# Optimization experiments

Measured on AMD Instinct MI355X. Metric: run time of the kernel, lower is better.

Reference implementation:

```python
import jax, jax.numpy as jnp
import numpy as np

N, D = 4096, 784

def _conv_relu(x, w, b):
    y = jax.lax.conv_general_dilated(x, w, window_strides=(1, 1), padding='SAME',
                                     dimension_numbers=('NHWC', 'HWIO', 'NHWC'))
    return jax.nn.relu(y + b)

def _maxpool2(x):
    return jax.lax.reduce_window(x, -jnp.inf, jax.lax.max,
                                 (1, 2, 2, 1), (1, 2, 2, 1), 'SAME')

def _encoder(x, cw1, cb1, cw2, cb2, cw3, cb3, dw, db):
    h = x.reshape(-1, 28, 28, 1)
    h = _maxpool2(_conv_relu(h, cw1, cb1))   # [N,14,14,32]
    h = _maxpool2(_conv_relu(h, cw2, cb2))   # [N,7,7,32]
    h = _conv_relu(h, cw3, cb3)              # [N,7,7,16]
    h = h.reshape(h.shape[0], -1)            # [N,784]
    return h @ dw + db                       # [N,16]

def _pairwise_dist(a):
    # Euclidean cdist via Gram trick; avoids the O(N^2 * D) broadcasted diff.
    sq = jnp.sum(a * a, axis=-1)
    d2 = sq[:, None] + sq[None, :] - 2.0 * (a @ a.T)
    return jnp.sqrt(jnp.maximum(d2, 1e-12))

def setup_inputs() -> dict:
    key = jax.random.key(0)
    ks = jax.random.split(key, 5)
    return {
        'x':   jax.random.uniform(ks[0], (N, D), dtype=jnp.float32),
        'cw1': jax.random.normal(ks[1], (3, 3, 1, 32), dtype=jnp.float32) * 0.1,
        'cb1': jnp.zeros((32,), jnp.float32),
        'cw2': jax.random.normal(ks[2], (3, 3, 32, 32), dtype=jnp.float32) * 0.05,
        'cb2': jnp.zeros((32,), jnp.float32),
        'cw3': jax.random.normal(ks[3], (3, 3, 32, 16), dtype=jnp.float32) * 0.05,
        'cb3': jnp.zeros((16,), jnp.float32),
        'dw':  jax.random.normal(ks[4], (D, 16), dtype=jnp.float32) * 0.05,
        'db':  jnp.zeros((16,), jnp.float32),
        'nnfactor': 64,
    }

def reference(x, cw1, cb1, cw2, cb2, cw3, cb3, dw, db, nnfactor):
    n = x.shape[0]
    k = n // nnfactor  # as in train_step
    encoded = _encoder(x, cw1, cb1, cw2, cb2, cw3, cb3, dw, db)
    # tensor_get_nearest (faithful: tf.nn.top_k takes LARGEST distances)
    d_ini = _pairwise_dist(x)                       # [N,N]
    vals_ini, idx = jax.lax.top_k(d_ini, k - 1)     # sorted descending
    vals_ini = vals_ini[:, 1:]                      # [N,k-2]
    idx = idx[:, 1:]
    d_enc = _pairwise_dist(encoded)                 # [N,N]
    vals_enc = jnp.take_along_axis(d_enc, idx, axis=1)
    multiple = jnp.mean(vals_ini / vals_enc)
    reduced = vals_enc * multiple
    # per-row custom loss: max squared error, then mean over batch
    losses = jnp.max(jnp.square(vals_ini - reduced), axis=1)  # [N]
    total_loss = jnp.sum(losses) / n
    return total_loss
```

## Files before the change

### kernel.cpp

```cpp
#include <hip/hip_runtime.h>
#include <math.h>

#define NN 4096
#define DIM 784
#define K62 62
#define CAP 160
#define NEED 80u

typedef __attribute__((ext_vector_type(8))) short bf16x8;
typedef __attribute__((ext_vector_type(4))) float f32x4;

__global__ __launch_bounds__(256) void k_sqnorm(const float* __restrict__ x, double* __restrict__ sqnd,
                                                float* __restrict__ sqnf) {
    int r = blockIdx.x * 4 + (threadIdx.x >> 6);
    int lane = threadIdx.x & 63;
    const float* xr = x + (size_t)r * DIM;
    double s = 0.0;
    for (int k = lane; k < DIM; k += 64) { double v = (double)xr[k]; s += v * v; }
    for (int o = 32; o > 0; o >>= 1) s += __shfl_down(s, o);
    if (lane == 0) { sqnd[r] = s; sqnf[r] = (float)s; }
}

#define F4C(v, i) ((i) == 0 ? (v).x : (i) == 1 ? (v).y : (i) == 2 ? (v).z : (v).w)

__device__ __forceinline__ unsigned short f2bf(float f) {
    unsigned u = __float_as_uint(f);
    return (unsigned short)((u + 0x7FFFu + ((u >> 16) & 1u)) >> 16);
}

__global__ __launch_bounds__(256) void k_tobf16(const float* __restrict__ x, unsigned short* __restrict__ xb) {
    int idx = blockIdx.x * 256 + threadIdx.x;
    int r = idx / 200;
    int c = (idx - r * 200) * 4;
    ushort4 o;
    if (c < DIM) {
        float4 v = *(const float4*)(x + (size_t)r * DIM + c);
        o.x = f2bf(v.x); o.y = f2bf(v.y); o.z = f2bf(v.z); o.w = f2bf(v.w);
    } else {
        o.x = 0; o.y = 0; o.z = 0; o.w = 0;
    }
    *(ushort4*)(xb + (size_t)r * 800 + c) = o;
}

__global__ __launch_bounds__(256, 2) void k_gram_mfma(const unsigned short* __restrict__ xb,
                                                      const float* __restrict__ sqnf,
                                                      unsigned short* __restrict__ Dm16) {
    __shared__ unsigned short Cs16[64 * 72];
    int t = threadIdx.x;
    int id = blockIdx.x;
    int bi = (int)((sqrtf(8.f * (float)id + 1.f) - 1.f) * 0.5f);
    while ((bi + 1) * (bi + 2) / 2 <= id) ++bi;
    while (bi * (bi + 1) / 2 > id) --bi;
    int bj = id - bi * (bi + 1) / 2;
    int i0 = bi * 128, j0 = bj * 128;
    int wv = t >> 6, ln = t & 63;
    int l16 = ln & 15, kg = ln >> 4;

    f32x4 acc[2][8];
    #pragma unroll
    for (int rt = 0; rt < 2; ++rt)
    #pragma unroll
    for (int ct = 0; ct < 8; ++ct)
    #pragma unroll
    for (int e = 0; e < 4; ++e) acc[rt][ct][e] = 0.f;

    const unsigned short* arow0 = xb + (size_t)(i0 + wv * 32 + l16) * 800 + kg * 8;
    const unsigned short* arow1 = arow0 + 16 * 800;
    const unsigned short* brow  = xb + (size_t)(j0 + l16) * 800 + kg * 8;

    for (int ks = 0; ks < 25; ++ks) {
        bf16x8 a0 = *(const bf16x8*)(arow0 + ks * 32);
        bf16x8 a1 = *(const bf16x8*)(arow1 + ks * 32);
        #pragma unroll
        for (int ct = 0; ct < 8; ++ct) {
            bf16x8 b = *(const bf16x8*)(brow + (size_t)ct * 16 * 800 + ks * 32);
            acc[0][ct] = __builtin_amdgcn_mfma_f32_16x16x32_bf16(a0, b, acc[0][ct], 0, 0, 0);
            acc[1][ct] = __builtin_amdgcn_mfma_f32_16x16x32_bf16(a1, b, acc[1][ct], 0, 0, 0);
        }
    }
    #pragma unroll
    for (int rt = 0; rt < 2; ++rt) {
        int gr0 = i0 + wv * 32 + rt * 16 + kg * 4;
        #pragma unroll
        for (int ct = 0; ct < 8; ++ct) {
            int gc = j0 + ct * 16 + l16;
            float sj = sqnf[gc];
            #pragma unroll
            for (int j = 0; j < 4; ++j) {
                float d2 = fmaxf(sqnf[gr0 + j] + sj - 2.f * acc[rt][ct][j], 1e-12f);
                Dm16[(size_t)(gr0 + j) * NN + gc] = (unsigned short)(__float_as_uint(d2) >> 16);
            }
        }
    }
    if (bi != bj) {
        for (int qr = 0; qr < 2; ++qr)
        for (int qc = 0; qc < 2; ++qc) {
            __syncthreads();
            #pragma unroll
            for (int g = 0; g < 2; ++g) {
                int idx = t + g * 256;
                int a = idx >> 3, c8 = idx & 7;
                uint4 v = *(const uint4*)&Dm16[(size_t)(i0 + qr * 64 + a) * NN + j0 + qc * 64 + c8 * 8];
                Cs16[(c8 * 8 + 0) * 72 + a] = (unsigned short)(v.x);
                Cs16[(c8 * 8 + 1) * 72 + a] = (unsigned short)(v.x >> 16);
                Cs16[(c8 * 8 + 2) * 72 + a] = (unsigned short)(v.y);
                Cs16[(c8 * 8 + 3) * 72 + a] = (unsigned short)(v.y >> 16);
                Cs16[(c8 * 8 + 4) * 72 + a] = (unsigned short)(v.z);
                Cs16[(c8 * 8 + 5) * 72 + a] = (unsigned short)(v.z >> 16);
                Cs16[(c8 * 8 + 6) * 72 + a] = (unsigned short)(v.w);
                Cs16[(c8 * 8 + 7) * 72 + a] = (unsigned short)(v.w >> 16);
            }
            __syncthreads();
            #pragma unroll
            for (int g = 0; g < 2; ++g) {
                int idx = t + g * 256;
                int a = idx >> 3, c8 = idx & 7;
                uint4 v = *(const uint4*)&Cs16[a * 72 + c8 * 8];
                *(uint4*)&Dm16[(size_t)(j0 + qc * 64 + a) * NN + i0 + qr * 64 + c8 * 8] = v;
            }
        }
    }
}

__global__ __launch_bounds__(256, 4) void k_encoder(const float* __restrict__ x,
    const float* __restrict__ cw1, const float* __restrict__ cb1,
    const float* __restrict__ cw2, const float* __restrict__ cb2,
    const float* __restrict__ cw3, const float* __restrict__ cb3,
    const float* __restrict__ dw, const float* __restrict__ db,
    double* __restrict__ Enc, double* __restrict__ esqd)
{
    __shared__ __align__(16) unsigned char SB[17408];
    float*  sb1  = (float*)(SB);
    float*  sb2  = (float*)(SB + 128);
    float*  sb3  = (float*)(SB + 256);
    float*  sdb  = (float*)(SB + 320);
    float*  scw1 = (float*)(SB + 384);
    float*  wq   = (float*)(SB + 1536);
    float*  simg = (float*)(SB + 6144);
    float*  h1q  = (float*)(SB + 9744);
    float*  wq3  = (float*)(SB + 1536);
    float*  h2s  = (float*)(SB + 6144);
    float*  c3   = (float*)(SB + 6144);
    double* red  = (double*)(SB + 14768);
    double* se   = (double*)(SB + 16816);

    int t = threadIdx.x;
    int n = blockIdx.x;
    for (int idx = t; idx < 1280; idx += 256) h1q[idx] = 0.f;
    for (int idx = t; idx < 900; idx += 256) simg[idx] = 0.f;
    __syncthreads();
    if (t < 196) {
        int row = t / 7, c4 = t % 7;
        float4 v = ((const float4*)(x + (size_t)n * DIM))[t];
        float* d = &simg[(row + 1) * 30 + 1 + c4 * 4];
        d[0] = v.x; d[1] = v.y; d[2] = v.z; d[3] = v.w;
    }
    for (int idx = t; idx < 288; idx += 256) scw1[idx] = cw1[idx];
    if (t < 32) { sb1[t] = cb1[t]; sb2[t] = cb2[t]; }
    if (t < 16) { sb3[t] = cb3[t]; sdb[t] = db[t]; }
    __syncthreads();

    int p2 = t >> 2, co8 = (t & 3) * 8;
    int py2 = p2 / 7, px2 = p2 % 7;
    int cbase = ((2 * py2) * 16 + 2 * px2) * 5;
    int ch1 = t & 3;
    float acc[4][8];
    if (t < 196) {
        #pragma unroll
        for (int pp = 0; pp < 4; ++pp)
        #pragma unroll
        for (int q = 0; q < 8; ++q) acc[pp][q] = sb2[co8 + q];
    }

    for (int oct = 0; oct < 8; ++oct) {
        __syncthreads();
        {
            int co = (oct << 2) + ch1;
            float wv[9];
            #pragma unroll
            for (int tp = 0; tp < 9; ++tp) wv[tp] = scw1[tp * 32 + co];
            float bias = sb1[co];
            for (int o = t; o < 784; o += 256) {
                int p = o >> 2;
                int py = p / 14, px = p % 14;
                float m = 0.f;
                #pragma unroll
                for (int dy = 0; dy < 2; ++dy)
                #pragma unroll
                for (int dx = 0; dx < 2; ++dx) {
                    const float* sp = &simg[(2 * py + dy + 1) * 30 + (2 * px + dx + 1)];
                    float a = bias;
                    a = fmaf(sp[-31], wv[0], a);
                    a = fmaf(sp[-30], wv[1], a);
                    a = fmaf(sp[-29], wv[2], a);
                    a = fmaf(sp[ -1], wv[3], a);
                    a = fmaf(sp[  0], wv[4], a);
                    a = fmaf(sp[  1], wv[5], a);
                    a = fmaf(sp[ 29], wv[6], a);
                    a = fmaf(sp[ 30], wv[7], a);
                    a = fmaf(sp[ 31], wv[8], a);
                    if (a < 0.f) a = 0.f;
                    if (a > m) m = a;
                }
                h1q[((py + 1) * 16 + (px + 1)) * 5 + ch1] = m;
            }
        }
        for (int w2 = t; w2 < 1152; w2 += 256) {
            int tap = w2 >> 7, k = w2 & 127;
            wq[w2] = cw2[tap * 1024 + oct * 128 + k];
        }
        __syncthreads();
        if (t < 196) {
            #pragma unroll
            for (int ky = 0; ky < 3; ++ky)
            #pragma unroll
            for (int kx = 0; kx < 3; ++kx) {
                const float* wb0 = &wq[(ky * 3 + kx) * 128 + co8];
                const float* hb = &h1q[cbase + (ky * 16 + kx) * 5];
                #pragma unroll
                for (int ci = 0; ci < 4; ++ci) {
                    float4 wA = *(const float4*)(wb0 + ci * 32);
                    float4 wB = *(const float4*)(wb0 + ci * 32 + 4);
                    float v00 = hb[ci];
                    float v01 = hb[5 + ci];
                    float v10 = hb[80 + ci];
                    float v11 = hb[85 + ci];
                    acc[0][0] = fmaf(v00, wA.x, acc[0][0]); acc[0][1] = fmaf(v00, wA.y, acc[0][1]);
                    acc[0][2] = fmaf(v00, wA.z, acc[0][2]); acc[0][3] = fmaf(v00, wA.w, acc[0][3]);
                    acc[0][4] = fmaf(v00, wB.x, acc[0][4]); acc[0][5] = fmaf(v00, wB.y, acc[0][5]);
                    acc[0][6] = fmaf(v00, wB.z, acc[0][6]); acc[0][7] = fmaf(v00, wB.w, acc[0][7]);
                    acc[1][0] = fmaf(v01, wA.x, acc[1][0]); acc[1][1] = fmaf(v01, wA.y, acc[1][1]);
                    acc[1][2] = fmaf(v01, wA.z, acc[1][2]); acc[1][3] = fmaf(v01, wA.w, acc[1][3]);
                    acc[1][4] = fmaf(v01, wB.x, acc[1][4]); acc[1][5] = fmaf(v01, wB.y, acc[1][5]);
                    acc[1][6] = fmaf(v01, wB.z, acc[1][6]); acc[1][7] = fmaf(v01, wB.w, acc[1][7]);
                    acc[2][0] = fmaf(v10, wA.x, acc[2][0]); acc[2][1] = fmaf(v10, wA.y, acc[2][1]);
                    acc[2][2] = fmaf(v10, wA.z, acc[2][2]); acc[2][3] = fmaf(v10, wA.w, acc[2][3]);
                    acc[2][4] = fmaf(v10, wB.x, acc[2][4]); acc[2][5] = fmaf(v10, wB.y, acc[2][5]);
                    acc[2][6] = fmaf(v10, wB.z, acc[2][6]); acc[2][7] = fmaf(v10, wB.w, acc[2][7]);
                    acc[3][0] = fmaf(v11, wA.x, acc[3][0]); acc[3][1] = fmaf(v11, wA.y, acc[3][1]);
                    acc[3][2] = fmaf(v11, wA.z, acc[3][2]); acc[3][3] = fmaf(v11, wA.w, acc[3][3]);
                    acc[3][4] = fmaf(v11, wB.x, acc[3][4]); acc[3][5] = fmaf(v11, wB.y, acc[3][5]);
                    acc[3][6] = fmaf(v11, wB.z, acc[3][6]); acc[3][7] = fmaf(v11, wB.w, acc[3][7]);
                }
            }
        }
    }
    __syncthreads();
    if (t < 196) {
        float mm[8];
        #pragma unroll
        for (int q = 0; q < 8; ++q) {
            float m = 0.f;
            #pragma unroll
            for (int pp = 0; pp < 4; ++pp) {
                float a = acc[pp][q];
                if (a < 0.f) a = 0.f;
                if (a > m) m = a;
            }
            mm[q] = m;
        }
        *(float4*)&h2s[p2 * 44 + co8]     = make_float4(mm[0], mm[1], mm[2], mm[3]);
        *(float4*)&h2s[p2 * 44 + co8 + 4] = make_float4(mm[4], mm[5], mm[6], mm[7]);
    }
    float a0 = 0.f, a1 = 0.f, a2 = 0.f, a3 = 0.f;
    int p3 = t >> 2, co4 = (t & 3) * 4;
    int py3 = p3 / 7, px3 = p3 % 7;
    if (t < 196) {
        a0 = sb3[co4]; a1 = sb3[co4 + 1];
        a2 = sb3[co4 + 2]; a3 = sb3[co4 + 3];
    }
    for (int qq = 0; qq < 4; ++qq) {
        __syncthreads();
        for (int w2 = t; w2 < 1152; w2 += 256) {
            int tap = w2 >> 7, k = w2 & 127;
            wq3[w2] = cw3[tap * 512 + qq * 128 + k];
        }
        __syncthreads();
        if (t < 196) {
            for (int ky = 0; ky < 3; ++ky) {
                int iy = py3 + ky - 1; if ((unsigned)iy >= 7u) continue;
                for (int kx = 0; kx < 3; ++kx) {
                    int ix = px3 + kx - 1; if ((unsigned)ix >= 7u) continue;
                    const float* hp = &h2s[(iy * 7 + ix) * 44 + qq * 8];
                    float4 h0 = *(const float4*)hp;
                    float4 h1 = *(const float4*)(hp + 4);
                    const float* wp = &wq3[(ky * 3 + kx) * 128 + co4];
                    #pragma unroll
                    for (int ci = 0; ci < 8; ++ci) {
                        float av = (ci < 4) ? F4C(h0, ci) : F4C(h1, ci - 4);
                        float4 wv = *(const float4*)(wp + ci * 16);
                        a0 = fmaf(av, wv.x, a0); a1 = fmaf(av, wv.y, a1);
                        a2 = fmaf(av, wv.z, a2); a3 = fmaf(av, wv.w, a3);
                    }
                }
            }
        }
    }
    __syncthreads();
    if (t < 196) {
        float r0 = a0 > 0.f ? a0 : 0.f, r1 = a1 > 0.f ? a1 : 0.f;
        float r2 = a2 > 0.f ? a2 : 0.f, r3 = a3 > 0.f ? a3 : 0.f;
        *(float4*)&c3[p3 * 16 + co4] = make_float4(r0, r1, r2, r3);
    }
    __syncthreads();
    {
        int part = t >> 4, o = t & 15, j0 = part * 49;
        double s = 0.0;
        for (int j = 0; j < 49; ++j) s = fma((double)c3[j0 + j], (double)dw[(size_t)(j0 + j) * 16 + o], s);
        red[part * 16 + o] = s;
    }
    __syncthreads();
    if (t < 16) {
        double e = (double)sdb[t];
        for (int q = 0; q < 16; ++q) e += red[q * 16 + t];
        Enc[(size_t)n * 16 + t] = e;
        se[t] = e;
    }
    __syncthreads();
    if (t == 0) {
        double s = 0.0;
        for (int q = 0; q < 16; ++q) s += se[q] * se[q];
        esqd[n] = s;
    }
}

__global__ __launch_bounds__(256) void k_topsel(const unsigned short* __restrict__ Dm16,
                                                const double* __restrict__ sqnd,
                                                const float* __restrict__ x,
                                                double* __restrict__ topvd, int* __restrict__ topi) {
    __shared__ float xi[DIM];
    __shared__ unsigned wsum[8];
    __shared__ int cj[CAP];
    __shared__ double cvd[CAP];
    __shared__ unsigned ncnt;
    int i = blockIdx.x, t = threadIdx.x;
    const unsigned* drow = (const unsigned*)(Dm16 + (size_t)i * NN);
    unsigned uk[8];
    #pragma unroll
    for (int s = 0; s < 8; ++s) {
        int wd = t + s * 256;
        unsigned u = drow[wd];
        if (2 * wd == i)     u &= 0xFFFF0000u;
        if (2 * wd + 1 == i) u &= 0x0000FFFFu;
        uk[s] = u;
    }
    if (t < 196) ((float4*)xi)[t] = ((const float4*)(x + (size_t)i * DIM))[t];
    if (t == 0) ncnt = 0;
    int lane = t & 63, w = t >> 6;
    unsigned lo = 0u, hi = 0xFFFFu;
    for (int it = 0; it < 16; ++it) {
        unsigned mid = (lo + hi + 1u) >> 1;
        unsigned cnt = 0;
        #pragma unroll
        for (int s = 0; s < 8; ++s) {
            cnt += ((uk[s] & 0xFFFFu) >= mid) ? 1u : 0u;
            cnt += ((uk[s] >> 16) >= mid) ? 1u : 0u;
        }
        #pragma unroll
        for (int off = 32; off > 0; off >>= 1) cnt += __shfl_down(cnt, off);
        if (lane == 0) wsum[(it & 1) * 4 + w] = cnt;
        __syncthreads();
        int bb = (it & 1) * 4;
        unsigned tot = wsum[bb] + wsum[bb + 1] + wsum[bb + 2] + wsum[bb + 3];
        if (tot >= NEED) lo = mid; else hi = mid - 1u;
    }
    unsigned prefix = lo;
    #pragma unroll
    for (int s = 0; s < 8; ++s) {
        int wd = t + s * 256;
        if ((uk[s] & 0xFFFFu) >= prefix) {
            unsigned p = atomicAdd(&ncnt, 1u);
            if (p < CAP) cj[p] = 2 * wd;
        }
        if ((uk[s] >> 16) >= prefix) {
            unsigned p = atomicAdd(&ncnt, 1u);
            if (p < CAP) cj[p] = 2 * wd + 1;
        }
    }
    __syncthreads();
    int ncand = min((int)ncnt, CAP);
    double sqi_d = sqnd[i];
    const float4* xi4 = (const float4*)xi;
    int g = t >> 4, gl = t & 15;
    for (int c = g; c < ncand; c += 16) {
        const float4* xj4 = (const float4*)(x + (size_t)cj[c] * DIM);
        double s = 0.0;
        for (int k = gl; k < 196; k += 16) {
            float4 a = xi4[k]; float4 b = xj4[k];
            s = fma((double)a.x, (double)b.x, s);
            s = fma((double)a.y, (double)b.y, s);
            s = fma((double)a.z, (double)b.z, s);
            s = fma((double)a.w, (double)b.w, s);
        }
        #pragma unroll
        for (int o = 8; o > 0; o >>= 1) s += __shfl_down(s, o, 16);
        if (gl == 0) cvd[c] = sqrt(fmax(sqi_d + sqnd[cj[c]] - 2.0 * s, 1e-12));
    }
    __syncthreads();
    if (t < ncand) {
        double v = cvd[t]; int jj = cj[t];
        int r = 0;
        for (int c2 = 0; c2 < ncand; ++c2) {
            double v2 = cvd[c2];
            if (v2 > v || (v2 == v && cj[c2] < jj)) ++r;
        }
        if (r >= 1 && r < 63) {
            topvd[(size_t)i * K62 + r - 1] = v;
            topi[(size_t)i * K62 + r - 1] = jj;
        }
    }
}

__global__ __launch_bounds__(256) void k_ratio(const double* __restrict__ Enc, const double* __restrict__ esqd,
                                               const double* __restrict__ topvd, const int* __restrict__ topi,
                                               double* __restrict__ vencd, double* __restrict__ Sp) {
    __shared__ double wp[4];
    int r = blockIdx.x * 4 + (threadIdx.x >> 6);
    int lane = threadIdx.x & 63, w = threadIdx.x >> 6;
    double ratio = 0.0;
    if (lane < K62) {
        int j = topi[(size_t)r * K62 + lane];
        const double* Er = Enc + (size_t)r * 16;
        const double* Ej = Enc + (size_t)j * 16;
        double dot = 0.0;
        #pragma unroll
        for (int q = 0; q < 16; ++q) dot = fma(Er[q], Ej[q], dot);
        double ve = sqrt(fmax(esqd[r] + esqd[j] - 2.0 * dot, 1e-12));
        vencd[(size_t)r * K62 + lane] = ve;
        ratio = topvd[(size_t)r * K62 + lane] / ve;
    }
    for (int o = 32; o > 0; o >>= 1) ratio += __shfl_down(ratio, o);
    if (lane == 0) wp[w] = ratio;
    __syncthreads();
    if (threadIdx.x == 0) Sp[blockIdx.x] = wp[0] + wp[1] + wp[2] + wp[3];
}

__global__ __launch_bounds__(256) void k_loss(const double* __restrict__ topvd, const double* __restrict__ vencd,
                                              const double* __restrict__ Sp, double* __restrict__ Lp) {
    __shared__ double wp[4];
    __shared__ double wq2[4];
    int t = threadIdx.x;
    int lane = t & 63, w = t >> 6;
    double sp = Sp[t] + Sp[t + 256] + Sp[t + 512] + Sp[t + 768];
    for (int o = 32; o > 0; o >>= 1) sp += __shfl_down(sp, o);
    if (lane == 0) wp[w] = sp;
    __syncthreads();
    double m = (wp[0] + wp[1] + wp[2] + wp[3]) * (1.0 / (4096.0 * 62.0));
    int r = blockIdx.x * 4 + w;
    double v = -1.0;
    if (lane < K62) {
        double d = topvd[(size_t)r * K62 + lane] - m * vencd[(size_t)r * K62 + lane];
        v = d * d;
    }
    for (int o = 32; o > 0; o >>= 1) { double ov = __shfl_down(v, o); v = (ov > v) ? ov : v; }
    if (lane == 0) wq2[w] = v;
    __syncthreads();
    if (t == 0) Lp[blockIdx.x] = wq2[0] + wq2[1] + wq2[2] + wq2[3];
}

__global__ __launch_bounds__(256) void k_final(const double* __restrict__ Lp, float* __restrict__ out) {
    __shared__ double wp[4];
    int t = threadIdx.x, lane = t & 63, w = t >> 6;
    double s = Lp[t] + Lp[t + 256] + Lp[t + 512] + Lp[t + 768];
    for (int o = 32; o > 0; o >>= 1) s += __shfl_down(s, o);
    if (lane == 0) wp[w] = s;
    __syncthreads();
    if (t == 0) out[0] = (float)((wp[0] + wp[1] + wp[2] + wp[3]) * (1.0 / 4096.0));
}

extern "C" void kernel_launch(void* const* d_in, const int* in_sizes, int n_in,
                              void* d_out, int out_size, void* d_ws, size_t ws_size,
                              hipStream_t stream) {
    const float* x   = (const float*)d_in[0];
    const float* cw1 = (const float*)d_in[1];
    const float* cb1 = (const float*)d_in[2];
    const float* cw2 = (const float*)d_in[3];
    const float* cb2 = (const float*)d_in[4];
    const float* cw3 = (const float*)d_in[5];
    const float* cb3 = (const float*)d_in[6];
    const float* dw  = (const float*)d_in[7];
    const float* db  = (const float*)d_in[8];

    char* wsb = (char*)d_ws;
    unsigned short* Dm16 = (unsigned short*)wsb;
    double* Enc   = (double*)(wsb + 33554432);
    double* esqd  = (double*)(wsb + 34078720);
    double* sqnd  = (double*)(wsb + 34111488);
    float*  sqnf  = (float*)(wsb + 34144256);
    double* topvd = (double*)(wsb + 34160640);
    double* vencd = (double*)(wsb + 36192256);
    int*    topi  = (int*)(wsb + 38223872);
    double* Sp    = (double*)(wsb + 39239680);
    double* Lp    = (double*)(wsb + 39247872);
    unsigned short* xb = (unsigned short*)(wsb + 39256064);
    float*  out   = (float*)d_out;

    k_sqnorm<<<1024, 256, 0, stream>>>(x, sqnd, sqnf);
    k_tobf16<<<3200, 256, 0, stream>>>(x, xb);
    k_gram_mfma<<<528, 256, 0, stream>>>(xb, sqnf, Dm16);
    k_encoder<<<4096, 256, 0, stream>>>(x, cw1, cb1, cw2, cb2, cw3, cb3, dw, db, Enc, esqd);
    k_topsel<<<4096, 256, 0, stream>>>(Dm16, sqnd, x, topvd, topi);
    k_ratio<<<1024, 256, 0, stream>>>(Enc, esqd, topvd, topi, vencd, Sp);
    k_loss<<<1024, 256, 0, stream>>>(topvd, vencd, Sp, Lp);
    k_final<<<1, 256, 0, stream>>>(Lp, out);
}
```

Before: 572.2 us.

## Fuse sqnorm with bf16 conversion and process two images per encoder block

Merges the squared-norm and bf16-conversion kernels into one pass over x, removing a launch and a second read of the input. The encoder now runs 512-thread blocks that each handle two images, sharing the staged conv2/conv3 weight loads between both halves and halving the number of weight copies into shared memory. This raises shared memory per block and makes each barrier wait on twice as many threads, which may reduce occupancy. The fused prep kernel uses scalar 2-byte stores in place of the earlier vectorized ushort4 stores.

```diff
diff --git a/kernel.cpp b/kernel.cpp
--- a/kernel.cpp
+++ b/kernel.cpp
@@ -10,37 +10,32 @@
 typedef __attribute__((ext_vector_type(8))) short bf16x8;
 typedef __attribute__((ext_vector_type(4))) float f32x4;
 
-__global__ __launch_bounds__(256) void k_sqnorm(const float* __restrict__ x, double* __restrict__ sqnd,
-                                                float* __restrict__ sqnf) {
+__device__ __forceinline__ unsigned short f2bf(float f) {
+    unsigned u = __float_as_uint(f);
+    return (unsigned short)((u + 0x7FFFu + ((u >> 16) & 1u)) >> 16);
+}
+
+__global__ __launch_bounds__(256) void k_prep(const float* __restrict__ x, double* __restrict__ sqnd,
+                                              float* __restrict__ sqnf, unsigned short* __restrict__ xb) {
     int r = blockIdx.x * 4 + (threadIdx.x >> 6);
     int lane = threadIdx.x & 63;
     const float* xr = x + (size_t)r * DIM;
+    unsigned short* xbr = xb + (size_t)r * 800;
     double s = 0.0;
-    for (int k = lane; k < DIM; k += 64) { double v = (double)xr[k]; s += v * v; }
+    for (int k = lane; k < 800; k += 64) {
+        if (k < DIM) {
+            float v = xr[k];
+            s = fma((double)v, (double)v, s);
+            xbr[k] = f2bf(v);
+        } else {
+            xbr[k] = 0;
+        }
+    }
     for (int o = 32; o > 0; o >>= 1) s += __shfl_down(s, o);
     if (lane == 0) { sqnd[r] = s; sqnf[r] = (float)s; }
 }
 
 #define F4C(v, i) ((i) == 0 ? (v).x : (i) == 1 ? (v).y : (i) == 2 ? (v).z : (v).w)
-
-__device__ __forceinline__ unsigned short f2bf(float f) {
-    unsigned u = __float_as_uint(f);
-    return (unsigned short)((u + 0x7FFFu + ((u >> 16) & 1u)) >> 16);
-}
-
-__global__ __launch_bounds__(256) void k_tobf16(const float* __restrict__ x, unsigned short* __restrict__ xb) {
-    int idx = blockIdx.x * 256 + threadIdx.x;
-    int r = idx / 200;
-    int c = (idx - r * 200) * 4;
-    ushort4 o;
-    if (c < DIM) {
-        float4 v = *(const float4*)(x + (size_t)r * DIM + c);
-        o.x = f2bf(v.x); o.y = f2bf(v.y); o.z = f2bf(v.z); o.w = f2bf(v.w);
-    } else {
-        o.x = 0; o.y = 0; o.z = 0; o.w = 0;
-    }
-    *(ushort4*)(xb + (size_t)r * 800 + c) = o;
-}
 
 __global__ __launch_bounds__(256, 2) void k_gram_mfma(const unsigned short* __restrict__ xb,
                                                       const float* __restrict__ sqnf,
@@ -122,50 +117,53 @@
     }
 }
 
-__global__ __launch_bounds__(256, 4) void k_encoder(const float* __restrict__ x,
+__global__ __launch_bounds__(512, 4) void k_encoder(const float* __restrict__ x,
     const float* __restrict__ cw1, const float* __restrict__ cb1,
     const float* __restrict__ cw2, const float* __restrict__ cb2,
     const float* __restrict__ cw3, const float* __restrict__ cb3,
     const float* __restrict__ dw, const float* __restrict__ db,
     double* __restrict__ Enc, double* __restrict__ esqd)
 {
-    __shared__ __align__(16) unsigned char SB[17408];
+    __shared__ __align__(16) unsigned char SB[23584];
     float*  sb1  = (float*)(SB);
     float*  sb2  = (float*)(SB + 128);
     float*  sb3  = (float*)(SB + 256);
     float*  sdb  = (float*)(SB + 320);
     float*  scw1 = (float*)(SB + 384);
     float*  wq   = (float*)(SB + 1536);
-    float*  simg = (float*)(SB + 6144);
-    float*  h1q  = (float*)(SB + 9744);
     float*  wq3  = (float*)(SB + 1536);
-    float*  h2s  = (float*)(SB + 6144);
-    float*  c3   = (float*)(SB + 6144);
-    double* red  = (double*)(SB + 14768);
-    double* se   = (double*)(SB + 16816);
 
     int t = threadIdx.x;
-    int n = blockIdx.x;
-    for (int idx = t; idx < 1280; idx += 256) h1q[idx] = 0.f;
-    for (int idx = t; idx < 900; idx += 256) simg[idx] = 0.f;
-    __syncthreads();
-    if (t < 196) {
-        int row = t / 7, c4 = t % 7;
-        float4 v = ((const float4*)(x + (size_t)n * DIM))[t];
+    int h = t >> 8, tl = t & 255;
+    unsigned char* RB = SB + 6144 + h * 8720;
+    float*  simg = (float*)RB;
+    float*  h1q  = (float*)(RB + 3600);
+    float*  h2s  = (float*)RB;
+    float*  c3   = (float*)RB;
+    double* red  = (double*)(RB + 3200);
+    double* se   = (double*)(RB + 5248);
+
+    int n = blockIdx.x * 2 + h;
+    for (int idx = tl; idx < 1280; idx += 256) h1q[idx] = 0.f;
+    for (int idx = tl; idx < 900; idx += 256) simg[idx] = 0.f;
+    __syncthreads();
+    if (tl < 196) {
+        int row = tl / 7, c4 = tl % 7;
+        float4 v = ((const float4*)(x + (size_t)n * DIM))[tl];
         float* d = &simg[(row + 1) * 30 + 1 + c4 * 4];
         d[0] = v.x; d[1] = v.y; d[2] = v.z; d[3] = v.w;
     }
-    for (int idx = t; idx < 288; idx += 256) scw1[idx] = cw1[idx];
+    for (int idx = t; idx < 288; idx += 512) scw1[idx] = cw1[idx];
     if (t < 32) { sb1[t] = cb1[t]; sb2[t] = cb2[t]; }
     if (t < 16) { sb3[t] = cb3[t]; sdb[t] = db[t]; }
     __syncthreads();
 
-    int p2 = t >> 2, co8 = (t & 3) * 8;
+    int p2 = tl >> 2, co8 = (tl & 3) * 8;
     int py2 = p2 / 7, px2 = p2 % 7;
     int cbase = ((2 * py2) * 16 + 2 * px2) * 5;
-    int ch1 = t & 3;
+    int ch1 = tl & 3;
     float acc[4][8];
-    if (t < 196) {
+    if (tl < 196) {
         #pragma unroll
         for (int pp = 0; pp < 4; ++pp)
         #pragma unroll
@@ -180,7 +178,7 @@
             #pragma unroll
             for (int tp = 0; tp < 9; ++tp) wv[tp] = scw1[tp * 32 + co];
             float bias = sb1[co];
-            for (int o = t; o < 784; o += 256) {
+            for (int o = tl; o < 784; o += 256) {
                 int p = o >> 2;
                 int py = p / 14, px = p % 14;
                 float m = 0.f;
@@ -205,12 +203,12 @@
                 h1q[((py + 1) * 16 + (px + 1)) * 5 + ch1] = m;
             }
         }
-        for (int w2 = t; w2 < 1152; w2 += 256) {
+        for (int w2 = t; w2 < 1152; w2 += 512) {
             int tap = w2 >> 7, k = w2 & 127;
             wq[w2] = cw2[tap * 1024 + oct * 128 + k];
         }
         __syncthreads();
-        if (t < 196) {
+        if (tl < 196) {
             #pragma unroll
             for (int ky = 0; ky < 3; ++ky)
             #pragma unroll
@@ -246,7 +244,7 @@
         }
     }
     __syncthreads();
-    if (t < 196) {
+    if (tl < 196) {
         float mm[8];
         #pragma unroll
         for (int q = 0; q < 8; ++q) {
@@ -263,20 +261,20 @@
         *(float4*)&h2s[p2 * 44 + co8 + 4] = make_float4(mm[4], mm[5], mm[6], mm[7]);
     }
     float a0 = 0.f, a1 = 0.f, a2 = 0.f, a3 = 0.f;
-    int p3 = t >> 2, co4 = (t & 3) * 4;
+    int p3 = tl >> 2, co4 = (tl & 3) * 4;
     int py3 = p3 / 7, px3 = p3 % 7;
-    if (t < 196) {
+    if (tl < 196) {
         a0 = sb3[co4]; a1 = sb3[co4 + 1];
         a2 = sb3[co4 + 2]; a3 = sb3[co4 + 3];
     }
     for (int qq = 0; qq < 4; ++qq) {
         __syncthreads();
-        for (int w2 = t; w2 < 1152; w2 += 256) {
+        for (int w2 = t; w2 < 1152; w2 += 512) {
             int tap = w2 >> 7, k = w2 & 127;
             wq3[w2] = cw3[tap * 512 + qq * 128 + k];
         }
         __syncthreads();
-        if (t < 196) {
+        if (tl < 196) {
             for (int ky = 0; ky < 3; ++ky) {
                 int iy = py3 + ky - 1; if ((unsigned)iy >= 7u) continue;
                 for (int kx = 0; kx < 3; ++kx) {
@@ -297,27 +295,27 @@
         }
     }
     __syncthreads();
-    if (t < 196) {
+    if (tl < 196) {
         float r0 = a0 > 0.f ? a0 : 0.f, r1 = a1 > 0.f ? a1 : 0.f;
         float r2 = a2 > 0.f ? a2 : 0.f, r3 = a3 > 0.f ? a3 : 0.f;
         *(float4*)&c3[p3 * 16 + co4] = make_float4(r0, r1, r2, r3);
     }
     __syncthreads();
     {
-        int part = t >> 4, o = t & 15, j0 = part * 49;
+        int part = tl >> 4, o = tl & 15, j0 = part * 49;
         double s = 0.0;
         for (int j = 0; j < 49; ++j) s = fma((double)c3[j0 + j], (double)dw[(size_t)(j0 + j) * 16 + o], s);
         red[part * 16 + o] = s;
     }
     __syncthreads();
-    if (t < 16) {
-        double e = (double)sdb[t];
-        for (int q = 0; q < 16; ++q) e += red[q * 16 + t];
-        Enc[(size_t)n * 16 + t] = e;
-        se[t] = e;
-    }
-    __syncthreads();
-    if (t == 0) {
+    if (tl < 16) {
+        double e = (double)sdb[tl];
+        for (int q = 0; q < 16; ++q) e += red[q * 16 + tl];
+        Enc[(size_t)n * 16 + tl] = e;
+        se[tl] = e;
+    }
+    __syncthreads();
+    if (tl == 0) {
         double s = 0.0;
         for (int q = 0; q < 16; ++q) s += se[q] * se[q];
         esqd[n] = s;
@@ -495,10 +493,9 @@
     unsigned short* xb = (unsigned short*)(wsb + 39256064);
     float*  out   = (float*)d_out;
 
-    k_sqnorm<<<1024, 256, 0, stream>>>(x, sqnd, sqnf);
-    k_tobf16<<<3200, 256, 0, stream>>>(x, xb);
+    k_prep<<<1024, 256, 0, stream>>>(x, sqnd, sqnf, xb);
     k_gram_mfma<<<528, 256, 0, stream>>>(xb, sqnf, Dm16);
-    k_encoder<<<4096, 256, 0, stream>>>(x, cw1, cb1, cw2, cb2, cw3, cb3, dw, db, Enc, esqd);
+    k_encoder<<<2048, 512, 0, stream>>>(x, cw1, cb1, cw2, cb2, cw3, cb3, dw, db, Enc, esqd);
     k_topsel<<<4096, 256, 0, stream>>>(Dm16, sqnd, x, topvd, topi);
     k_ratio<<<1024, 256, 0, stream>>>(Enc, esqd, topvd, topi, vencd, Sp);
     k_loss<<<1024, 256, 0, stream>>>(topvd, vencd, Sp, Lp);
```

Measured after the change: 592.8 us. 3.6% more time.
